# Kernel optimization log

Measured on AMD Instinct MI355X. Metric: run time of the kernel, lower is better.

## Reference

```python
import jax, jax.numpy as jnp
import numpy as np
import math

L, S, N, E, H = 2048, 2048, 2, 512, 8
D = E // H


def setup_inputs() -> dict:
    key = jax.random.key(0)
    ks = jax.random.split(key, 12)
    scale = 1.0 / math.sqrt(E)
    return {
        "query": jax.random.normal(ks[0], (L, N, E), jnp.float32),
        "key": jax.random.normal(ks[1], (S, N, E), jnp.float32),
        "value": jax.random.normal(ks[2], (S, N, E), jnp.float32),
        "attn_bias": jax.random.normal(ks[3], (L, S), jnp.float32),
        "Wq": jax.random.normal(ks[4], (E, E), jnp.float32) * scale,
        "bq": jnp.zeros((E,), jnp.float32),
        "Wk": jax.random.normal(ks[5], (E, E), jnp.float32) * scale,
        "bk": jnp.zeros((E,), jnp.float32),
        "Wv": jax.random.normal(ks[6], (E, E), jnp.float32) * scale,
        "bv": jnp.zeros((E,), jnp.float32),
        "Wo": jax.random.normal(ks[7], (E, E), jnp.float32) * scale,
        "bo": jnp.zeros((E,), jnp.float32),
    }


def reference(query, key, value, attn_bias, Wq, bq, Wk, bk, Wv, bv, Wo, bo):
    # Linear projections (nn.Linear: x @ W.T + b)
    Q = (query @ Wq.T + bq).reshape(L, N, H, D)
    K = (key @ Wk.T + bk).reshape(S, N, H, D)
    V = (value @ Wv.T + bv).reshape(S, N, H, D)
    # scores: [H, N, L, S]
    scores = jnp.einsum("lnhd,snhd->hnls", Q, K) / math.sqrt(D)
    scores = scores + attn_bias[None, None, :, :]
    attn_weights = jax.nn.softmax(scores, axis=-1)  # dropout p=0 / eval
    # attention output: [L, N, H, D] -> [L, N, E]
    attn_out = jnp.einsum("hnls,snhd->lnhd", attn_weights, V).reshape(L, N, E)
    attn_out = attn_out @ Wo.T + bo
    return attn_out, attn_weights.reshape(H * N, L, S)
```

## Files before the change

kernel.cpp:

```cpp
#include <hip/hip_runtime.h>
#include <hip/hip_bf16.h>
#include <math.h>

#define L_SEQ 2048
#define S_SEQ 2048
#define N_B 2
#define E_DIM 512
#define H_HEADS 8
#define D_HEAD 64
#define M_ROWS (L_SEQ * N_B)
#define BH (H_HEADS * N_B)

typedef __attribute__((ext_vector_type(8))) short bf16x8;
typedef __attribute__((ext_vector_type(4))) float f32x4;

#define MFMA(a, b, c) __builtin_amdgcn_mfma_f32_16x16x32_bf16((a), (b), (c), 0, 0, 0)

__device__ __forceinline__ short f2bf(float v) {
    union { __hip_bfloat16 h; short s; } u;
    u.h = __float2bfloat16(v);
    return u.s;
}
__device__ __forceinline__ float bf2f(short s) {
    union { __hip_bfloat16 h; short t; } u;
    u.t = s;
    return __bfloat162float(u.h);
}
__device__ __forceinline__ void cvt8_hl(const float4& a, const float4& b, bf16x8& h, bf16x8& l) {
    float v[8] = {a.x, a.y, a.z, a.w, b.x, b.y, b.z, b.w};
#pragma unroll
    for (int i = 0; i < 8; ++i) {
        short hh = f2bf(v[i]);
        h[i] = hh;
        l[i] = f2bf(v[i] - bf2f(hh));
    }
}
__device__ __forceinline__ bf16x8 cvt8_h(const float4& a, const float4& b) {
    float v[8] = {a.x, a.y, a.z, a.w, b.x, b.y, b.z, b.w};
    bf16x8 h;
#pragma unroll
    for (int i = 0; i < 8; ++i) h[i] = f2bf(v[i]);
    return h;
}

__global__ __launch_bounds__(256) void fill_kernel(float4* __restrict__ p, int n4) {
    const float4 z = {0.f, 0.f, 0.f, 0.f};
    for (int i = blockIdx.x * 256 + threadIdx.x; i < n4; i += gridDim.x * 256) p[i] = z;
}

__global__ __launch_bounds__(256) void split_kernel(const float* __restrict__ in,
                                                    short* __restrict__ hi,
                                                    short* __restrict__ lo, int n8) {
    const int i = blockIdx.x * 256 + threadIdx.x;
    if (i >= n8) return;
    const float4* p = (const float4*)(in + (size_t)i * 8);
    bf16x8 h, l;
    cvt8_hl(p[0], p[1], h, l);
    *(bf16x8*)(hi + (size_t)i * 8) = h;
    *(bf16x8*)(lo + (size_t)i * 8) = l;
}

__global__ __launch_bounds__(256) void proj_kernel(
    const short* __restrict__ Xh, const short* __restrict__ Xl,
    const short* __restrict__ Wh, const short* __restrict__ Wl,
    const float* __restrict__ bias, short* __restrict__ outH,
    short* __restrict__ outL, int writeLo) {
    const int bn = blockIdx.x * 64;
    const int bm = blockIdx.y * 64;
    const int tid = threadIdx.x;
    const int wave = tid >> 6, lane = tid & 63;
    const int m16 = lane & 15, q = lane >> 4;

    const short* pAh = Xh + (size_t)(bm + wave * 16 + m16) * E_DIM;
    const short* pAl = Xl + (size_t)(bm + wave * 16 + m16) * E_DIM;

    f32x4 acc[4] = {};
    for (int k0 = 0; k0 < E_DIM; k0 += 32) {
        const bf16x8 ah = *(const bf16x8*)(pAh + k0 + q * 8);
        const bf16x8 al = *(const bf16x8*)(pAl + k0 + q * 8);
#pragma unroll
        for (int j = 0; j < 4; ++j) {
            const size_t bo = (size_t)(bn + j * 16 + m16) * E_DIM + k0 + q * 8;
            const bf16x8 bh_ = *(const bf16x8*)(Wh + bo);
            const bf16x8 bl_ = *(const bf16x8*)(Wl + bo);
            acc[j] = MFMA(ah, bh_, acc[j]);
            acc[j] = MFMA(ah, bl_, acc[j]);
            acc[j] = MFMA(al, bh_, acc[j]);
        }
    }

#pragma unroll
    for (int j = 0; j < 4; ++j) {
        const int e = bn + j * 16 + m16;
        const int h = e >> 6, d = e & 63;
        const float be = bias[e];
#pragma unroll
        for (int r = 0; r < 4; ++r) {
            const int row = bm + wave * 16 + q * 4 + r;
            const int l = row >> 1, nb = row & 1;
            const float v = acc[j][r] + be;
            const size_t idx = ((size_t)(h * 2 + nb) * L_SEQ + l) * D_HEAD + d;
            const short hi = f2bf(v);
            outH[idx] = hi;
            if (writeLo) outL[idx] = f2bf(v - bf2f(hi));
        }
    }
}

__global__ __launch_bounds__(256) void vtrans_kernel(const short* __restrict__ Vb,
                                                     short* __restrict__ Vt) {
    __shared__ short tile[64][65];
    const int s0 = blockIdx.x * 64;
    const int bh = blockIdx.y;
    const int t = threadIdx.x;
    const int r = t >> 2, seg = (t & 3) * 16;
    const bf16x8* p = (const bf16x8*)(Vb + ((size_t)bh * S_SEQ + s0 + r) * D_HEAD + seg);
    bf16x8 v0 = p[0], v1 = p[1];
#pragma unroll
    for (int i = 0; i < 8; ++i) {
        tile[r][seg + i] = v0[i];
        tile[r][seg + 8 + i] = v1[i];
    }
    __syncthreads();
    bf16x8 o0, o1;
#pragma unroll
    for (int i = 0; i < 8; ++i) {
        o0[i] = tile[seg + i][r];
        o1[i] = tile[seg + 8 + i][r];
    }
    bf16x8* po = (bf16x8*)(Vt + ((size_t)bh * D_HEAD + r) * S_SEQ + s0 + seg);
    po[0] = o0;
    po[1] = o1;
}

__global__ __launch_bounds__(512) void scores_pv_kernel(
    const short* __restrict__ Qh, const short* __restrict__ Ql,
    const short* __restrict__ Kh, const short* __restrict__ Kl,
    const short* __restrict__ Vt, const float* __restrict__ bias,
    float* __restrict__ wout, short* __restrict__ ctx) {
    const int bh = blockIdx.y;
    const int l0 = blockIdx.x * 16;
    const int tid = threadIdx.x;
    const int wave = tid >> 6, lane = tid & 63;
    const int m16 = lane & 15, q = lane >> 4;
    const int sbase = wave * 256;

    __shared__ float LMAX[8][16], LSUM[8][16];
    __shared__ __align__(16) float SM_T[8][32][17];
    __shared__ __align__(16) float OB[8][16][65];

    const size_t qoff = ((size_t)bh * L_SEQ + l0 + m16) * D_HEAD;
    bf16x8 aH[2], aL[2];
#pragma unroll
    for (int ks = 0; ks < 2; ++ks) {
        aH[ks] = *(const bf16x8*)(Qh + qoff + ks * 32 + q * 8);
        aL[ks] = *(const bf16x8*)(Ql + qoff + ks * 32 + q * 8);
    }

    f32x4 C[16] = {};
#pragma unroll
    for (int t = 0; t < 16; ++t) {
        const size_t koff = ((size_t)bh * S_SEQ + sbase + t * 16 + m16) * D_HEAD;
#pragma unroll
        for (int ks = 0; ks < 2; ++ks) {
            const bf16x8 kh = *(const bf16x8*)(Kh + koff + ks * 32 + q * 8);
            const bf16x8 kl = *(const bf16x8*)(Kl + koff + ks * 32 + q * 8);
            C[t] = MFMA(aH[ks], kh, C[t]);
            C[t] = MFMA(aH[ks], kl, C[t]);
            C[t] = MFMA(aL[ks], kh, C[t]);
        }
    }

    const int row0 = l0 + q * 4;
#pragma unroll
    for (int r = 0; r < 4; ++r) {
        const float* brow = bias + (size_t)(row0 + r) * S_SEQ + sbase + m16;
#pragma unroll
        for (int t = 0; t < 16; ++t) C[t][r] = C[t][r] * 0.125f + brow[t * 16];
    }

    float mx[4] = {-INFINITY, -INFINITY, -INFINITY, -INFINITY};
#pragma unroll
    for (int t = 0; t < 16; ++t)
#pragma unroll
        for (int r = 0; r < 4; ++r) mx[r] = fmaxf(mx[r], C[t][r]);
#pragma unroll
    for (int d = 1; d < 16; d <<= 1)
#pragma unroll
        for (int r = 0; r < 4; ++r) mx[r] = fmaxf(mx[r], __shfl_xor(mx[r], d, 64));
    if (m16 == 0) {
#pragma unroll
        for (int r = 0; r < 4; ++r) LMAX[wave][q * 4 + r] = mx[r];
    }
    __syncthreads();
    float M[4];
#pragma unroll
    for (int r = 0; r < 4; ++r) {
        float v = -INFINITY;
#pragma unroll
        for (int w = 0; w < 8; ++w) v = fmaxf(v, LMAX[w][q * 4 + r]);
        M[r] = v;
    }

    float sm[4] = {};
#pragma unroll
    for (int t = 0; t < 16; ++t)
#pragma unroll
        for (int r = 0; r < 4; ++r) {
            const float e = __expf(C[t][r] - M[r]);
            C[t][r] = e;
            sm[r] += e;
        }
#pragma unroll
    for (int d = 1; d < 16; d <<= 1)
#pragma unroll
        for (int r = 0; r < 4; ++r) sm[r] += __shfl_xor(sm[r], d, 64);
    if (m16 == 0) {
#pragma unroll
        for (int r = 0; r < 4; ++r) LSUM[wave][q * 4 + r] = sm[r];
    }
    __syncthreads();
#pragma unroll
    for (int r = 0; r < 4; ++r) {
        float s = 0.f;
#pragma unroll
        for (int w = 0; w < 8; ++w) s += LSUM[w][q * 4 + r];
        const float inv = 1.0f / s;
        float* orow = wout + ((size_t)bh * L_SEQ + row0 + r) * S_SEQ + sbase + m16;
#pragma unroll
        for (int t = 0; t < 16; ++t) {
            C[t][r] *= inv;
            orow[t * 16] = C[t][r];
        }
    }

    f32x4 O[4] = {};
    float (*T)[17] = SM_T[wave];
    for (int c = 0; c < 8; ++c) {
        __syncthreads();
#pragma unroll
        for (int r = 0; r < 4; ++r) {
            T[m16][q * 4 + r]      = C[2 * c][r];
            T[16 + m16][q * 4 + r] = C[2 * c + 1][r];
        }
        __syncthreads();
        bf16x8 a;
#pragma unroll
        for (int j = 0; j < 8; ++j) a[j] = f2bf(T[q * 8 + j][m16]);
        const int scol = sbase + c * 32;
#pragma unroll
        for (int j = 0; j < 4; ++j) {
            const bf16x8 b =
                *(const bf16x8*)(Vt + ((size_t)bh * D_HEAD + j * 16 + m16) * S_SEQ + scol + q * 8);
            O[j] = MFMA(a, b, O[j]);
        }
    }

    __syncthreads();
#pragma unroll
    for (int j = 0; j < 4; ++j)
#pragma unroll
        for (int r = 0; r < 4; ++r) OB[wave][q * 4 + r][j * 16 + m16] = O[j][r];
    __syncthreads();

    const int h = bh >> 1, n = bh & 1;
#pragma unroll
    for (int u = 0; u < 2; ++u) {
        const int idx = tid + u * 512;
        const int row = idx >> 6, d = idx & 63;
        float s = 0.f;
#pragma unroll
        for (int w = 0; w < 8; ++w) s += OB[w][row][d];
        ctx[(size_t)((l0 + row) * N_B + n) * E_DIM + h * D_HEAD + d] = f2bf(s);
    }
}

__global__ __launch_bounds__(256) void oproj_kernel(const short* __restrict__ ctx,
                                                    const float* __restrict__ W,
                                                    const float* __restrict__ bias,
                                                    float* __restrict__ out) {
    __shared__ __align__(16) short Bh[64 * 40];
    const int bn = blockIdx.x * 64;
    const int bm = blockIdx.y * 64;
    const int tid = threadIdx.x;
    const int wave = tid >> 6, lane = tid & 63;
    const int m16 = lane & 15, q = lane >> 4;
    const int srow = tid >> 2, sk = (tid & 3) * 8;

    f32x4 acc[4] = {};
    for (int k0 = 0; k0 < E_DIM; k0 += 32) {
        {
            const float4* pb = (const float4*)(W + (size_t)(bn + srow) * E_DIM + k0 + sk);
            *(bf16x8*)&Bh[srow * 40 + sk] = cvt8_h(pb[0], pb[1]);
        }
        __syncthreads();
        const bf16x8 a = *(const bf16x8*)(ctx + (size_t)(bm + wave * 16 + m16) * E_DIM + k0 + q * 8);
#pragma unroll
        for (int j = 0; j < 4; ++j) {
            const bf16x8 b = *(const bf16x8*)&Bh[(j * 16 + m16) * 40 + q * 8];
            acc[j] = MFMA(a, b, acc[j]);
        }
        __syncthreads();
    }
#pragma unroll
    for (int j = 0; j < 4; ++j) {
        const int e = bn + j * 16 + m16;
        const float be = bias[e];
#pragma unroll
        for (int r = 0; r < 4; ++r)
            out[(size_t)(bm + wave * 16 + q * 4 + r) * E_DIM + e] = acc[j][r] + be;
    }
}

extern "C" void kernel_launch(void* const* d_in, const int* in_sizes, int n_in,
                              void* d_out, int out_size, void* d_ws, size_t ws_size,
                              hipStream_t stream) {
    const float* query = (const float*)d_in[0];
    const float* key   = (const float*)d_in[1];
    const float* value = (const float*)d_in[2];
    const float* bias  = (const float*)d_in[3];
    const float* Wq    = (const float*)d_in[4];
    const float* bq    = (const float*)d_in[5];
    const float* Wk    = (const float*)d_in[6];
    const float* bk    = (const float*)d_in[7];
    const float* Wv    = (const float*)d_in[8];
    const float* bv    = (const float*)d_in[9];
    const float* Wo    = (const float*)d_in[10];
    const float* bo    = (const float*)d_in[11];

    float* out0 = (float*)d_out;
    float* wgt  = out0 + (size_t)M_ROWS * E_DIM;

    short* wsS = (short*)d_ws;
    const size_t buf = (size_t)BH * L_SEQ * D_HEAD;
    short* Qh  = wsS + 0 * buf;
    short* Ql  = wsS + 1 * buf;
    short* Kh  = wsS + 2 * buf;
    short* Kl  = wsS + 3 * buf;
    short* Vh  = wsS + 4 * buf;
    short* Vt  = wsS + 5 * buf;   short* Xl = Vt;
    short* ctx = wsS + 6 * buf;   short* Xh = ctx;

    const size_t wb = (size_t)E_DIM * E_DIM;
    const size_t wgtElems = (size_t)BH * L_SEQ * S_SEQ;
    short* WhT = (short*)wgt + 2 * wgtElems - 2 * wb;
    short* WlT = WhT + wb;

    const int nW8 = (int)(wb / 8);
    const int nX8 = (int)((size_t)M_ROWS * E_DIM / 8);
    const dim3 gproj(E_DIM / 64, M_ROWS / 64);

    fill_kernel<<<2048, 256, 0, stream>>>((float4*)d_ws, (int)(7 * buf * sizeof(short) / 16));

    split_kernel<<<nX8 / 256, 256, 0, stream>>>(query, Xh, Xl, nX8);
    split_kernel<<<nW8 / 256, 256, 0, stream>>>(Wq, WhT, WlT, nW8);
    proj_kernel<<<gproj, 256, 0, stream>>>(Xh, Xl, WhT, WlT, bq, Qh, Ql, 1);
    split_kernel<<<nX8 / 256, 256, 0, stream>>>(key, Xh, Xl, nX8);
    split_kernel<<<nW8 / 256, 256, 0, stream>>>(Wk, WhT, WlT, nW8);
    proj_kernel<<<gproj, 256, 0, stream>>>(Xh, Xl, WhT, WlT, bk, Kh, Kl, 1);
    split_kernel<<<nX8 / 256, 256, 0, stream>>>(value, Xh, Xl, nX8);
    split_kernel<<<nW8 / 256, 256, 0, stream>>>(Wv, WhT, WlT, nW8);
    proj_kernel<<<gproj, 256, 0, stream>>>(Xh, Xl, WhT, WlT, bv, Vh, (short*)wgt, 0);

    vtrans_kernel<<<dim3(S_SEQ / 64, BH), 256, 0, stream>>>(Vh, Vt);

    scores_pv_kernel<<<dim3(L_SEQ / 16, BH), 512, 0, stream>>>(Qh, Ql, Kh, Kl, Vt, bias, wgt, ctx);

    oproj_kernel<<<gproj, 256, 0, stream>>>(ctx, Wo, bo, out0);
}
```

Before: 652.7 us.

## Batch QKV projections, stage GEMM tiles in LDS, split PV into separate kernel

Merges the three Q/K/V split and projection launches into batched kernels indexed by blockIdx, and stages A/B tiles through shared memory in the projection GEMM. Moves the P·V product out of the scores kernel into its own kernel, which re-reads the fp32 attention weights from global memory instead of keeping them in registers. Pre-splits Wo to bf16 instead of converting it inside the output projection. The result is fewer launches and better GEMM reuse, at the cost of an extra read of the large weights matrix (about 512MB).

```diff
diff --git a/kernel.cpp b/kernel.cpp
--- a/kernel.cpp
+++ b/kernel.cpp
@@ -46,6 +46,24 @@
 __global__ __launch_bounds__(256) void fill_kernel(float4* __restrict__ p, int n4) {
     const float4 z = {0.f, 0.f, 0.f, 0.f};
     for (int i = blockIdx.x * 256 + threadIdx.x; i < n4; i += gridDim.x * 256) p[i] = z;
+}
+
+__global__ __launch_bounds__(256) void split3_kernel(
+    const float* __restrict__ in0, const float* __restrict__ in1, const float* __restrict__ in2,
+    short* __restrict__ h0, short* __restrict__ l0,
+    short* __restrict__ h1, short* __restrict__ l1,
+    short* __restrict__ h2, short* __restrict__ l2, int n8) {
+    const int z = blockIdx.y;
+    const float* in = (z == 0) ? in0 : (z == 1) ? in1 : in2;
+    short* hi = (z == 0) ? h0 : (z == 1) ? h1 : h2;
+    short* lo = (z == 0) ? l0 : (z == 1) ? l1 : l2;
+    const int i = blockIdx.x * 256 + threadIdx.x;
+    if (i >= n8) return;
+    const float4* p = (const float4*)(in + (size_t)i * 8);
+    bf16x8 h, l;
+    cvt8_hl(p[0], p[1], h, l);
+    *(bf16x8*)(hi + (size_t)i * 8) = h;
+    *(bf16x8*)(lo + (size_t)i * 8) = l;
 }
 
 __global__ __launch_bounds__(256) void split_kernel(const float* __restrict__ in,
@@ -60,33 +78,58 @@
     *(bf16x8*)(lo + (size_t)i * 8) = l;
 }
 
-__global__ __launch_bounds__(256) void proj_kernel(
-    const short* __restrict__ Xh, const short* __restrict__ Xl,
-    const short* __restrict__ Wh, const short* __restrict__ Wl,
-    const float* __restrict__ bias, short* __restrict__ outH,
-    short* __restrict__ outL, int writeLo) {
+__global__ __launch_bounds__(256) void proj_qkv3_kernel(
+    const short* __restrict__ Xh0, const short* __restrict__ Xl0,
+    const short* __restrict__ Xh1, const short* __restrict__ Xl1,
+    const short* __restrict__ Xh2, const short* __restrict__ Xl2,
+    const short* __restrict__ Wh0, const short* __restrict__ Wl0,
+    const short* __restrict__ Wh1, const short* __restrict__ Wl1,
+    const short* __restrict__ Wh2, const short* __restrict__ Wl2,
+    const float* __restrict__ b0, const float* __restrict__ b1, const float* __restrict__ b2,
+    short* __restrict__ oH0, short* __restrict__ oL0,
+    short* __restrict__ oH1, short* __restrict__ oL1,
+    short* __restrict__ oH2, short* __restrict__ oL2) {
+    const int z = blockIdx.z;
+    const short* Xh = (z == 0) ? Xh0 : (z == 1) ? Xh1 : Xh2;
+    const short* Xl = (z == 0) ? Xl0 : (z == 1) ? Xl1 : Xl2;
+    const short* Wh = (z == 0) ? Wh0 : (z == 1) ? Wh1 : Wh2;
+    const short* Wl = (z == 0) ? Wl0 : (z == 1) ? Wl1 : Wl2;
+    const float* bias = (z == 0) ? b0 : (z == 1) ? b1 : b2;
+    short* outH = (z == 0) ? oH0 : (z == 1) ? oH1 : oH2;
+    short* outL = (z == 0) ? oL0 : (z == 1) ? oL1 : oL2;
+    const int writeLo = (z < 2);
+
+    __shared__ __align__(16) short Ah[64 * 40], Al[64 * 40], Bh[64 * 40], Bl[64 * 40];
     const int bn = blockIdx.x * 64;
     const int bm = blockIdx.y * 64;
     const int tid = threadIdx.x;
     const int wave = tid >> 6, lane = tid & 63;
     const int m16 = lane & 15, q = lane >> 4;
-
-    const short* pAh = Xh + (size_t)(bm + wave * 16 + m16) * E_DIM;
-    const short* pAl = Xl + (size_t)(bm + wave * 16 + m16) * E_DIM;
+    const int srow = tid >> 2, sk = (tid & 3) * 8;
 
     f32x4 acc[4] = {};
+
     for (int k0 = 0; k0 < E_DIM; k0 += 32) {
-        const bf16x8 ah = *(const bf16x8*)(pAh + k0 + q * 8);
-        const bf16x8 al = *(const bf16x8*)(pAl + k0 + q * 8);
+        {
+            const size_t ax = (size_t)(bm + srow) * E_DIM + k0 + sk;
+            const size_t bx = (size_t)(bn + srow) * E_DIM + k0 + sk;
+            *(bf16x8*)&Ah[srow * 40 + sk] = *(const bf16x8*)(Xh + ax);
+            *(bf16x8*)&Al[srow * 40 + sk] = *(const bf16x8*)(Xl + ax);
+            *(bf16x8*)&Bh[srow * 40 + sk] = *(const bf16x8*)(Wh + bx);
+            *(bf16x8*)&Bl[srow * 40 + sk] = *(const bf16x8*)(Wl + bx);
+        }
+        __syncthreads();
+        const bf16x8 ah = *(const bf16x8*)&Ah[(wave * 16 + m16) * 40 + q * 8];
+        const bf16x8 al = *(const bf16x8*)&Al[(wave * 16 + m16) * 40 + q * 8];
 #pragma unroll
         for (int j = 0; j < 4; ++j) {
-            const size_t bo = (size_t)(bn + j * 16 + m16) * E_DIM + k0 + q * 8;
-            const bf16x8 bh_ = *(const bf16x8*)(Wh + bo);
-            const bf16x8 bl_ = *(const bf16x8*)(Wl + bo);
+            const bf16x8 bh_ = *(const bf16x8*)&Bh[(j * 16 + m16) * 40 + q * 8];
+            const bf16x8 bl_ = *(const bf16x8*)&Bl[(j * 16 + m16) * 40 + q * 8];
             acc[j] = MFMA(ah, bh_, acc[j]);
             acc[j] = MFMA(ah, bl_, acc[j]);
             acc[j] = MFMA(al, bh_, acc[j]);
         }
+        __syncthreads();
     }
 
 #pragma unroll
@@ -133,11 +176,10 @@
     po[1] = o1;
 }
 
-__global__ __launch_bounds__(512) void scores_pv_kernel(
+__global__ __launch_bounds__(512) void scores_sm_kernel(
     const short* __restrict__ Qh, const short* __restrict__ Ql,
     const short* __restrict__ Kh, const short* __restrict__ Kl,
-    const short* __restrict__ Vt, const float* __restrict__ bias,
-    float* __restrict__ wout, short* __restrict__ ctx) {
+    const float* __restrict__ bias, float* __restrict__ wout) {
     const int bh = blockIdx.y;
     const int l0 = blockIdx.x * 16;
     const int tid = threadIdx.x;
@@ -146,8 +188,6 @@
     const int sbase = wave * 256;
 
     __shared__ float LMAX[8][16], LSUM[8][16];
-    __shared__ __align__(16) float SM_T[8][32][17];
-    __shared__ __align__(16) float OB[8][16][65];
 
     const size_t qoff = ((size_t)bh * L_SEQ + l0 + m16) * D_HEAD;
     bf16x8 aH[2], aL[2];
@@ -233,50 +273,41 @@
             orow[t * 16] = C[t][r];
         }
     }
-
-    f32x4 O[4] = {};
-    float (*T)[17] = SM_T[wave];
-    for (int c = 0; c < 8; ++c) {
-        __syncthreads();
+}
+
+__global__ __launch_bounds__(256) void pv_kernel(const float* __restrict__ P,
+                                                 const short* __restrict__ Vt,
+                                                 short* __restrict__ ctx) {
+    const int bm = blockIdx.x * 64;
+    const int bh = blockIdx.y;
+    const int tid = threadIdx.x;
+    const int wave = tid >> 6, lane = tid & 63;
+    const int m16 = lane & 15, q = lane >> 4;
+
+    const float* pA = P + ((size_t)bh * L_SEQ + bm + wave * 16 + m16) * S_SEQ;
+    f32x4 acc[4] = {};
+    for (int s0 = 0; s0 < S_SEQ; s0 += 32) {
+        const float4* pa = (const float4*)(pA + s0 + q * 8);
+        const bf16x8 a = cvt8_h(pa[0], pa[1]);
+#pragma unroll
+        for (int j = 0; j < 4; ++j) {
+            const bf16x8 b = *(const bf16x8*)(Vt + ((size_t)bh * D_HEAD + j * 16 + m16) * S_SEQ +
+                                              s0 + q * 8);
+            acc[j] = MFMA(a, b, acc[j]);
+        }
+    }
+    const int h = bh >> 1, n = bh & 1;
+#pragma unroll
+    for (int j = 0; j < 4; ++j)
 #pragma unroll
         for (int r = 0; r < 4; ++r) {
-            T[m16][q * 4 + r]      = C[2 * c][r];
-            T[16 + m16][q * 4 + r] = C[2 * c + 1][r];
-        }
-        __syncthreads();
-        bf16x8 a;
-#pragma unroll
-        for (int j = 0; j < 8; ++j) a[j] = f2bf(T[q * 8 + j][m16]);
-        const int scol = sbase + c * 32;
-#pragma unroll
-        for (int j = 0; j < 4; ++j) {
-            const bf16x8 b =
-                *(const bf16x8*)(Vt + ((size_t)bh * D_HEAD + j * 16 + m16) * S_SEQ + scol + q * 8);
-            O[j] = MFMA(a, b, O[j]);
-        }
-    }
-
-    __syncthreads();
-#pragma unroll
-    for (int j = 0; j < 4; ++j)
-#pragma unroll
-        for (int r = 0; r < 4; ++r) OB[wave][q * 4 + r][j * 16 + m16] = O[j][r];
-    __syncthreads();
-
-    const int h = bh >> 1, n = bh & 1;
-#pragma unroll
-    for (int u = 0; u < 2; ++u) {
-        const int idx = tid + u * 512;
-        const int row = idx >> 6, d = idx & 63;
-        float s = 0.f;
-#pragma unroll
-        for (int w = 0; w < 8; ++w) s += OB[w][row][d];
-        ctx[(size_t)((l0 + row) * N_B + n) * E_DIM + h * D_HEAD + d] = f2bf(s);
-    }
+            const int l = bm + wave * 16 + q * 4 + r;
+            ctx[(size_t)(l * N_B + n) * E_DIM + h * D_HEAD + j * 16 + m16] = f2bf(acc[j][r]);
+        }
 }
 
 __global__ __launch_bounds__(256) void oproj_kernel(const short* __restrict__ ctx,
-                                                    const float* __restrict__ W,
+                                                    const short* __restrict__ Wh,
                                                     const float* __restrict__ bias,
                                                     float* __restrict__ out) {
     __shared__ __align__(16) short Bh[64 * 40];
@@ -290,8 +321,8 @@
     f32x4 acc[4] = {};
     for (int k0 = 0; k0 < E_DIM; k0 += 32) {
         {
-            const float4* pb = (const float4*)(W + (size_t)(bn + srow) * E_DIM + k0 + sk);
-            *(bf16x8*)&Bh[srow * 40 + sk] = cvt8_h(pb[0], pb[1]);
+            *(bf16x8*)&Bh[srow * 40 + sk] =
+                *(const bf16x8*)(Wh + (size_t)(bn + srow) * E_DIM + k0 + sk);
         }
         __syncthreads();
         const bf16x8 a = *(const bf16x8*)(ctx + (size_t)(bm + wave * 16 + m16) * E_DIM + k0 + q * 8);
@@ -338,33 +369,49 @@
     short* Kh  = wsS + 2 * buf;
     short* Kl  = wsS + 3 * buf;
     short* Vh  = wsS + 4 * buf;
-    short* Vt  = wsS + 5 * buf;   short* Xl = Vt;
-    short* ctx = wsS + 6 * buf;   short* Xh = ctx;
-
+    short* Vt  = wsS + 5 * buf;
+    short* ctx = wsS + 6 * buf;
+
+    const size_t Xe = (size_t)M_ROWS * E_DIM;
     const size_t wb = (size_t)E_DIM * E_DIM;
     const size_t wgtElems = (size_t)BH * L_SEQ * S_SEQ;
-    short* WhT = (short*)wgt + 2 * wgtElems - 2 * wb;
-    short* WlT = WhT + wb;
+    const size_t totalS = 6 * Xe + 6 * wb;
+    short* scr = (short*)wgt + 2 * wgtElems - totalS;
+    short* Xqh = scr + 0 * Xe; short* Xql = scr + 1 * Xe;
+    short* Xkh = scr + 2 * Xe; short* Xkl = scr + 3 * Xe;
+    short* Xvh = scr + 4 * Xe; short* Xvl = scr + 5 * Xe;
+    short* Wqh = scr + 6 * Xe;  short* Wql = Wqh + wb;
+    short* Wkh = Wql + wb;      short* Wkl = Wkh + wb;
+    short* Wvh = Wkl + wb;      short* Wvl = Wvh + wb;
+
+    short* Woh = Qh;
+    short* Wol = Qh + wb;
 
     const int nW8 = (int)(wb / 8);
-    const int nX8 = (int)((size_t)M_ROWS * E_DIM / 8);
+    const int nX8 = (int)(Xe / 8);
+    const dim3 gproj3(E_DIM / 64, M_ROWS / 64, 3);
     const dim3 gproj(E_DIM / 64, M_ROWS / 64);
 
     fill_kernel<<<2048, 256, 0, stream>>>((float4*)d_ws, (int)(7 * buf * sizeof(short) / 16));
 
-    split_kernel<<<nX8 / 256, 256, 0, stream>>>(query, Xh, Xl, nX8);
-    split_kernel<<<nW8 / 256, 256, 0, stream>>>(Wq, WhT, WlT, nW8);
-    proj_kernel<<<gproj, 256, 0, stream>>>(Xh, Xl, WhT, WlT, bq, Qh, Ql, 1);
-    split_kernel<<<nX8 / 256, 256, 0, stream>>>(key, Xh, Xl, nX8);
-    split_kernel<<<nW8 / 256, 256, 0, stream>>>(Wk, WhT, WlT, nW8);
-    proj_kernel<<<gproj, 256, 0, stream>>>(Xh, Xl, WhT, WlT, bk, Kh, Kl, 1);
-    split_kernel<<<nX8 / 256, 256, 0, stream>>>(value, Xh, Xl, nX8);
-    split_kernel<<<nW8 / 256, 256, 0, stream>>>(Wv, WhT, WlT, nW8);
-    proj_kernel<<<gproj, 256, 0, stream>>>(Xh, Xl, WhT, WlT, bv, Vh, (short*)wgt, 0);
+    split3_kernel<<<dim3(nX8 / 256, 3), 256, 0, stream>>>(
+        query, key, value, Xqh, Xql, Xkh, Xkl, Xvh, Xvl, nX8);
+    split3_kernel<<<dim3(nW8 / 256, 3), 256, 0, stream>>>(
+        Wq, Wk, Wv, Wqh, Wql, Wkh, Wkl, Wvh, Wvl, nW8);
+
+    proj_qkv3_kernel<<<gproj3, 256, 0, stream>>>(
+        Xqh, Xql, Xkh, Xkl, Xvh, Xvl,
+        Wqh, Wql, Wkh, Wkl, Wvh, Wvl,
+        bq, bk, bv,
+        Qh, Ql, Kh, Kl, Vh, (short*)wgt);
 
     vtrans_kernel<<<dim3(S_SEQ / 64, BH), 256, 0, stream>>>(Vh, Vt);
 
-    scores_pv_kernel<<<dim3(L_SEQ / 16, BH), 512, 0, stream>>>(Qh, Ql, Kh, Kl, Vt, bias, wgt, ctx);
-
-    oproj_kernel<<<gproj, 256, 0, stream>>>(ctx, Wo, bo, out0);
-}
+    scores_sm_kernel<<<dim3(L_SEQ / 16, BH), 512, 0, stream>>>(Qh, Ql, Kh, Kl, bias, wgt);
+
+    split_kernel<<<nW8 / 256, 256, 0, stream>>>(Wo, Woh, Wol, nW8);
+
+    pv_kernel<<<dim3(L_SEQ / 64, BH), 256, 0, stream>>>(wgt, Vt, ctx);
+
+    oproj_kernel<<<gproj, 256, 0, stream>>>(ctx, Woh, bo, out0);
+}
```

Result: faster. 619.3 us (-5.1%).
